# Kernel tuning notes

Hardware: AMD Instinct MI355X
Metric: run time of the kernel (lower is better)

## Reference

```python
import jax, jax.numpy as jnp
import numpy as np
from jax import lax

EMBED_DIM = 512
HIDDEN_DIM = 256
OUT_DIM = HIDDEN_DIM // 2
BATCH = 32
SEQ = 4096
THRESHOLD = 1.0
DECAY = 0.95
REFRACTORY = 2.0


def setup_inputs() -> dict:
    key = jax.random.key(0)
    k1, k2, k3 = jax.random.split(key, 3)
    x = jax.random.normal(k1, (BATCH, SEQ, EMBED_DIM), dtype=jnp.float32)
    input_weights = jax.random.normal(k2, (EMBED_DIM, HIDDEN_DIM), dtype=jnp.float32) * 0.1
    hidden_weights = jax.random.normal(k3, (HIDDEN_DIM, OUT_DIM), dtype=jnp.float32) * 0.1
    return {"x": x, "input_weights": input_weights, "hidden_weights": hidden_weights}


def reference(x, input_weights, hidden_weights):
    B, S, D = x.shape
    H = input_weights.shape[1]
    dt = x.dtype
    # batch-mean then project all timesteps at once: [S, H]
    currents = jnp.einsum('sd,dh->sh', x.mean(0), input_weights)

    def step(carry, ic):
        mem, refr = carry
        active = (refr <= 0).astype(dt)
        mem = DECAY * mem + ic * active
        spikes = (mem >= THRESHOLD).astype(dt)
        mem = mem * (1.0 - spikes)
        refr = jnp.maximum(refr - 1.0, 0.0) + spikes * REFRACTORY
        return (mem, refr), spikes

    init = (jnp.zeros((H,), dt), jnp.zeros((H,), dt))
    _, spikes = lax.scan(step, init, currents)  # spikes: [S, H]
    out = spikes @ hidden_weights               # [S, OUT]
    out_mean = out.mean(0)                      # mean over timesteps
    # original repeats the (batch-independent) output across the batch
    return jnp.broadcast_to(out_mean, (B, out_mean.shape[0]))
```

## Files before the change

kernel.cpp:

```cpp
#include <hip/hip_runtime.h>
#include <stdint.h>


#define S_LEN 4096
#define D_DIM 512
#define H_DIM 256
#define O_DIM 128
#define B_SZ  32

#define NPROD 1024
#define CH    64
#define NCH   (S_LEN / CH)
#define ROWS  (CH / 4)

typedef const __attribute__((address_space(1))) void  glob_void;
typedef       __attribute__((address_space(3))) void  lds_void;

#define LIF_STEP(IC) {                          \
    float ict = sp2 ? 0.f : (IC);               \
    float tt  = fmaf(0.95f, u, ict);            \
    u   = sp1 ? 0.f : tt;                       \
    bool sp = (u >= 1.0f);                      \
    cnt += sp ? 1 : 0;                          \
    sp2 = sp1; sp1 = sp; }

#define ACC4(A, V) { A.x += V.x; A.y += V.y; A.z += V.z; A.w += V.w; }

__global__ __launch_bounds__(256)
void snn_produce(const float4* __restrict__ x4,
                 const float*  __restrict__ iw,
                 float4*       __restrict__ cur4) {
    __shared__ float4 xm[4 * (D_DIM / 4)];
    const int t   = threadIdx.x;
    const int r2  = t >> 7;
    const int d4  = t & 127;
    const int h   = t;
    const float inv = 1.0f / (float)B_SZ;
    const size_t bstr = (size_t)S_LEN * (D_DIM / 4);

    const int f  = (int)blockIdx.x;
    const int s0 = 4 * f;

    float4 a0 = make_float4(0.f, 0.f, 0.f, 0.f);
    float4 a1 = make_float4(0.f, 0.f, 0.f, 0.f);
    const float4* xb = x4 + (size_t)(s0 + r2) * (D_DIM / 4) + d4;
    for (int b = 0; b < B_SZ; b += 4) {
        const float4* p = xb + (size_t)b * bstr;
        float4 v00 = p[0],            v01 = p[2 * (D_DIM / 4)];
        float4 v10 = p[bstr],         v11 = p[bstr + 2 * (D_DIM / 4)];
        float4 v20 = p[2 * bstr],     v21 = p[2 * bstr + 2 * (D_DIM / 4)];
        float4 v30 = p[3 * bstr],     v31 = p[3 * bstr + 2 * (D_DIM / 4)];
        ACC4(a0, v00); ACC4(a0, v10); ACC4(a0, v20); ACC4(a0, v30);
        ACC4(a1, v01); ACC4(a1, v11); ACC4(a1, v21); ACC4(a1, v31);
    }
    a0.x *= inv; a0.y *= inv; a0.z *= inv; a0.w *= inv;
    a1.x *= inv; a1.y *= inv; a1.z *= inv; a1.w *= inv;
    xm[r2 * (D_DIM / 4) + d4]       = a0;
    xm[(r2 + 2) * (D_DIM / 4) + d4] = a1;
    __syncthreads();

    float acc2[4] = {0.f, 0.f, 0.f, 0.f};
    for (int d4i = 0; d4i < D_DIM / 4; ++d4i) {
        const int d = d4i * 4;
        float w0 = iw[(d + 0) * H_DIM + h];
        float w1 = iw[(d + 1) * H_DIM + h];
        float w2 = iw[(d + 2) * H_DIM + h];
        float w3 = iw[(d + 3) * H_DIM + h];
        #pragma unroll
        for (int r = 0; r < 4; ++r) {
            float4 xv = xm[r * (D_DIM / 4) + d4i];
            acc2[r] += xv.x * w0 + xv.y * w1 + xv.z * w2 + xv.w * w3;
        }
    }
    cur4[(size_t)f * H_DIM + h] = make_float4(acc2[0], acc2[1], acc2[2], acc2[3]);
}

__global__ __launch_bounds__(64)
void snn_scan(const float4* __restrict__ cur4,
              const float*  __restrict__ hw,
              float*        __restrict__ out) {
    __shared__ __attribute__((aligned(16))) float4 lbuf[2][ROWS * 64];
    __shared__ float cl[64];
    const int lane  = threadIdx.x;
    const int hbase = (int)blockIdx.x * 64;

    auto stage = [&](int c) {
        #pragma unroll
        for (int r = 0; r < ROWS; ++r) {
            const float4* g = cur4 + (size_t)(c * ROWS + r) * H_DIM + hbase + lane;
            __builtin_amdgcn_global_load_lds((glob_void*)g,
                                             (lds_void*)&lbuf[c & 1][r * 64 + lane],
                                             16, 0, 0);
        }
    };

    float u = 0.f;
    int   cnt = 0;
    bool  sp1 = false, sp2 = false;

    stage(0);
    for (int c = 0; c < NCH; ++c) {
        if (c + 1 < NCH) {
            stage(c + 1);
            asm volatile("s_waitcnt vmcnt(16)" ::: "memory");
        } else {
            asm volatile("s_waitcnt vmcnt(0)" ::: "memory");
        }
        __builtin_amdgcn_sched_barrier(0);

        const float4* lb = lbuf[c & 1];
        float4 v[ROWS];
        #pragma unroll
        for (int r = 0; r < ROWS; ++r) v[r] = lb[r * 64 + lane];
        __builtin_amdgcn_sched_barrier(0);

        #pragma unroll
        for (int r = 0; r < ROWS; ++r) {
            LIF_STEP(v[r].x); LIF_STEP(v[r].y); LIF_STEP(v[r].z); LIF_STEP(v[r].w);
        }
    }

    __syncthreads();
    cl[lane] = (float)cnt;
    __syncthreads();
    float a0 = 0.f, a1 = 0.f;
    #pragma unroll 8
    for (int k = 0; k < 64; ++k) {
        float c = cl[k];
        const float* w = hw + (size_t)(hbase + k) * O_DIM;
        a0 = fmaf(c, w[lane], a0);
        a1 = fmaf(c, w[lane + 64], a1);
    }
    a0 *= (1.0f / (float)S_LEN);
    a1 *= (1.0f / (float)S_LEN);
    for (int b = 0; b < B_SZ; ++b) {
        atomicAdd(out + b * O_DIM + lane,      a0);
        atomicAdd(out + b * O_DIM + lane + 64, a1);
    }
}

extern "C" void kernel_launch(void* const* d_in, const int* in_sizes, int n_in,
                              void* d_out, int out_size, void* d_ws, size_t ws_size,
                              hipStream_t stream) {
    const float4* x4 = (const float4*)d_in[0];
    const float*  iw = (const float*) d_in[1];
    const float*  hw = (const float*) d_in[2];
    float* out   = (float*)d_out;
    float4* cur4 = (float4*)d_ws;

    (void)hipMemsetAsync(out, 0, B_SZ * O_DIM * sizeof(float), stream);
    hipLaunchKernelGGL(snn_produce, dim3(NPROD), dim3(256), 0, stream,
                       x4, iw, cur4);
    hipLaunchKernelGGL(snn_scan, dim3(4), dim3(64), 0, stream,
                       cur4, hw, out);
}
```

Before: 468.3 us.

## Stream batch slabs via async LDS loads and triple-buffer scan chunks

```diff
diff --git a/kernel.cpp b/kernel.cpp
--- a/kernel.cpp
+++ b/kernel.cpp
@@ -30,33 +30,53 @@
 void snn_produce(const float4* __restrict__ x4,
                  const float*  __restrict__ iw,
                  float4*       __restrict__ cur4) {
-    __shared__ float4 xm[4 * (D_DIM / 4)];
-    const int t   = threadIdx.x;
-    const int r2  = t >> 7;
-    const int d4  = t & 127;
-    const int h   = t;
+    __shared__ __attribute__((aligned(16))) float4 slab[4][512];
+    __shared__ float4 xm[512];
+    const int t    = threadIdx.x;
+    const int w    = t >> 6;
+    const int lane = t & 63;
+    const int r2   = t >> 7;
+    const int d4   = t & 127;
+    const int h    = t;
     const float inv = 1.0f / (float)B_SZ;
     const size_t bstr = (size_t)S_LEN * (D_DIM / 4);
 
-    const int f  = (int)blockIdx.x;
-    const int s0 = 4 * f;
+    const int f = (int)blockIdx.x;
+    const float4* sbase = x4 + (size_t)(4 * f) * (D_DIM / 4);
+
+    auto issue = [&](int b) {
+        const float4* g = sbase + (size_t)b * bstr + w * 128 + lane;
+        __builtin_amdgcn_global_load_lds((glob_void*)g,
+                                         (lds_void*)&slab[b & 3][w * 128 + lane],
+                                         16, 0, 0);
+        __builtin_amdgcn_global_load_lds((glob_void*)(g + 64),
+                                         (lds_void*)&slab[b & 3][w * 128 + 64 + lane],
+                                         16, 0, 0);
+    };
+
+    issue(0); issue(1); issue(2);
 
     float4 a0 = make_float4(0.f, 0.f, 0.f, 0.f);
     float4 a1 = make_float4(0.f, 0.f, 0.f, 0.f);
-    const float4* xb = x4 + (size_t)(s0 + r2) * (D_DIM / 4) + d4;
-    for (int b = 0; b < B_SZ; b += 4) {
-        const float4* p = xb + (size_t)b * bstr;
-        float4 v00 = p[0],            v01 = p[2 * (D_DIM / 4)];
-        float4 v10 = p[bstr],         v11 = p[bstr + 2 * (D_DIM / 4)];
-        float4 v20 = p[2 * bstr],     v21 = p[2 * bstr + 2 * (D_DIM / 4)];
-        float4 v30 = p[3 * bstr],     v31 = p[3 * bstr + 2 * (D_DIM / 4)];
-        ACC4(a0, v00); ACC4(a0, v10); ACC4(a0, v20); ACC4(a0, v30);
-        ACC4(a1, v01); ACC4(a1, v11); ACC4(a1, v21); ACC4(a1, v31);
+    for (int b = 0; b < B_SZ; ++b) {
+        if (b < B_SZ - 2)      asm volatile("s_waitcnt vmcnt(4)" ::: "memory");
+        else if (b == B_SZ - 2) asm volatile("s_waitcnt vmcnt(2)" ::: "memory");
+        else                    asm volatile("s_waitcnt vmcnt(0)" ::: "memory");
+        __builtin_amdgcn_s_barrier();
+        __builtin_amdgcn_sched_barrier(0);
+        if (b + 3 < B_SZ) issue(b + 3);
+        float4 v0 = slab[b & 3][r2 * 128 + d4];
+        float4 v1 = slab[b & 3][(r2 + 2) * 128 + d4];
+        ACC4(a0, v0);
+        ACC4(a1, v1);
+        asm volatile("s_waitcnt lgkmcnt(0)" ::: "memory");
+        __builtin_amdgcn_sched_barrier(0);
     }
+
     a0.x *= inv; a0.y *= inv; a0.z *= inv; a0.w *= inv;
     a1.x *= inv; a1.y *= inv; a1.z *= inv; a1.w *= inv;
-    xm[r2 * (D_DIM / 4) + d4]       = a0;
-    xm[(r2 + 2) * (D_DIM / 4) + d4] = a1;
+    xm[r2 * 128 + d4]       = a0;
+    xm[(r2 + 2) * 128 + d4] = a1;
     __syncthreads();
 
     float acc2[4] = {0.f, 0.f, 0.f, 0.f};
@@ -68,7 +88,7 @@
         float w3 = iw[(d + 3) * H_DIM + h];
         #pragma unroll
         for (int r = 0; r < 4; ++r) {
-            float4 xv = xm[r * (D_DIM / 4) + d4i];
+            float4 xv = xm[r * 128 + d4i];
             acc2[r] += xv.x * w0 + xv.y * w1 + xv.z * w2 + xv.w * w3;
         }
     }
@@ -79,17 +99,17 @@
 void snn_scan(const float4* __restrict__ cur4,
               const float*  __restrict__ hw,
               float*        __restrict__ out) {
-    __shared__ __attribute__((aligned(16))) float4 lbuf[2][ROWS * 64];
+    __shared__ __attribute__((aligned(16))) float4 lbuf[3][ROWS * 64];
     __shared__ float cl[64];
     const int lane  = threadIdx.x;
     const int hbase = (int)blockIdx.x * 64;
 
-    auto stage = [&](int c) {
+    auto stage = [&](int c, int idx) {
         #pragma unroll
         for (int r = 0; r < ROWS; ++r) {
             const float4* g = cur4 + (size_t)(c * ROWS + r) * H_DIM + hbase + lane;
             __builtin_amdgcn_global_load_lds((glob_void*)g,
-                                             (lds_void*)&lbuf[c & 1][r * 64 + lane],
+                                             (lds_void*)&lbuf[idx][r * 64 + lane],
                                              16, 0, 0);
         }
     };
@@ -98,17 +118,23 @@
     int   cnt = 0;
     bool  sp1 = false, sp2 = false;
 
-    stage(0);
+    stage(0, 0);
+    stage(1, 1);
+    int rd = 0, st = 2;
     for (int c = 0; c < NCH; ++c) {
-        if (c + 1 < NCH) {
-            stage(c + 1);
+        if (c + 2 < NCH) {
+            stage(c + 2, st);
+            st = (st == 2) ? 0 : st + 1;
+            asm volatile("s_waitcnt vmcnt(32)" ::: "memory");
+        } else if (c + 1 < NCH) {
             asm volatile("s_waitcnt vmcnt(16)" ::: "memory");
         } else {
             asm volatile("s_waitcnt vmcnt(0)" ::: "memory");
         }
         __builtin_amdgcn_sched_barrier(0);
 
-        const float4* lb = lbuf[c & 1];
+        const float4* lb = &lbuf[rd][0];
+        rd = (rd == 2) ? 0 : rd + 1;
         float4 v[ROWS];
         #pragma unroll
         for (int r = 0; r < ROWS; ++r) v[r] = lb[r * 64 + lane];
```

Result: no change. 467.5 us (-0.2%).
